# Optimization experiments

Measured on AMD Instinct MI355X. Metric: run time of the kernel, lower is better.

The kernel has to match this reference:

```python
import jax, jax.numpy as jnp
import numpy as np

N_EXPERTS = 8
TOP_K = 2

# NOTE: dropout is treated as identity (inference/eval mode), matching
# nn.Dropout in eval(). gate_logits returned is post-softmax, exactly as in
# the torch code (it overwrites gate_logits with F.softmax output).

def setup_inputs() -> dict:
    key = jax.random.key(0)
    k1, k2, k3, k4 = jax.random.split(key, 4)
    B, T, S = 32, 512, 512
    x = jax.random.normal(k1, (B, T, S), dtype=jnp.float32)
    gate_w = jax.random.normal(k2, (N_EXPERTS, S), dtype=jnp.float32) * (1.0 / np.sqrt(S))
    expert_w = jax.random.normal(k3, (N_EXPERTS, S, S), dtype=jnp.float32) * (1.0 / np.sqrt(S))
    expert_b = jax.random.normal(k4, (N_EXPERTS, S), dtype=jnp.float32) * 0.01
    return {"x": x, "gate_w": gate_w, "expert_w": expert_w, "expert_b": expert_b}


def reference(x, gate_w, expert_w, expert_b):
    # Gating: Linear(seq_len -> n_experts, no bias) then softmax over experts
    logits = jnp.einsum('bti,ei->bte', x, gate_w)          # [B,T,E]
    gates = jax.nn.softmax(logits, axis=-1)                # [B,T,E]
    # top-k routing weights
    w, sel = jax.lax.top_k(gates, TOP_K)                   # [B,T,K], [B,T,K]
    # dense combine weights: zero except at selected experts
    comb = jnp.sum(jax.nn.one_hot(sel, N_EXPERTS, dtype=x.dtype) * w[..., None], axis=-2)  # [B,T,E]
    # all-expert linear outputs (XLA fuses the weighted combine)
    expert_out = jnp.einsum('bti,eoi->bteo', x, expert_w) + expert_b[None, None]  # [B,T,E,S]
    out = jnp.einsum('bte,bteo->bto', comb, expert_out)    # [B,T,S]
    out = jax.nn.relu(out)
    return (out, gates)
```

## Files before the change

### kernel.cpp

```cpp
#include <hip/hip_runtime.h>
#include <stdint.h>

#define NT 16384
#define SDIM 512
#define NE 8
#define BM 128
#define BN 128
#define BK 32
#define NSTEP (SDIM / BK)
#define NPAIR 28
#define MAX_TILES 156
#define GEMM_GRID (MAX_TILES * 4)

typedef __attribute__((ext_vector_type(8))) short short8v;
typedef __attribute__((ext_vector_type(8))) unsigned short ushort8v;
typedef __attribute__((ext_vector_type(4))) float f32x4;

#define GLOAD_LDS16(gp, lp) __builtin_amdgcn_global_load_lds( \
    (const __attribute__((address_space(1))) uint32_t*)(gp), \
    (__attribute__((address_space(3))) uint32_t*)(lp), 16, 0, 0)

__device__ __forceinline__ unsigned short f2bf(float f) {
  uint32_t x = __float_as_uint(f);
  x = (x + 0x7FFFu + ((x >> 16) & 1u)) >> 16;
  return (unsigned short)x;
}

__global__ __launch_bounds__(256) void convw_kernel(const float* __restrict__ w,
                                                    unsigned short* __restrict__ wb) {
  int i = (blockIdx.x * 256 + threadIdx.x) * 8;
  const float4* p = (const float4*)(w + i);
  float4 a = p[0], b = p[1];
  ushort8v u;
  u[0] = f2bf(a.x); u[1] = f2bf(a.y); u[2] = f2bf(a.z); u[3] = f2bf(a.w);
  u[4] = f2bf(b.x); u[5] = f2bf(b.y); u[6] = f2bf(b.z); u[7] = f2bf(b.w);
  *(ushort8v*)(wb + i) = u;
}

__global__ __launch_bounds__(256) void gate_kernel(
    const float* __restrict__ x, const float* __restrict__ gw,
    unsigned short* __restrict__ xb, float* __restrict__ gates_out,
    float* __restrict__ wts, int* __restrict__ sels) {
  int lane = threadIdx.x & 63;
  int wv = threadIdx.x >> 6;

  float4 ga[NE], gb[NE];
#pragma unroll
  for (int e = 0; e < NE; e++) {
    const float4* g4 = (const float4*)(gw + e * SDIM + lane * 8);
    ga[e] = g4[0]; gb[e] = g4[1];
  }

  int tbase = blockIdx.x * 16 + wv * 4;
#pragma unroll 1
  for (int i = 0; i < 4; i++) {
    int t = tbase + i;
    const float* xr = x + (size_t)t * SDIM;
    float4 xa = ((const float4*)xr)[lane * 2];
    float4 xbv = ((const float4*)xr)[lane * 2 + 1];

    ushort8v u;
    u[0] = f2bf(xa.x); u[1] = f2bf(xa.y); u[2] = f2bf(xa.z); u[3] = f2bf(xa.w);
    u[4] = f2bf(xbv.x); u[5] = f2bf(xbv.y); u[6] = f2bf(xbv.z); u[7] = f2bf(xbv.w);
    *(ushort8v*)(xb + (size_t)t * SDIM + lane * 8) = u;

    double part[NE];
#pragma unroll
    for (int e = 0; e < NE; e++) {
      double s;
      s  = (double)xa.x * ga[e].x;  s += (double)xa.y * ga[e].y;
      s += (double)xa.z * ga[e].z;  s += (double)xa.w * ga[e].w;
      s += (double)xbv.x * gb[e].x; s += (double)xbv.y * gb[e].y;
      s += (double)xbv.z * gb[e].z; s += (double)xbv.w * gb[e].w;
      part[e] = s;
    }
#pragma unroll
    for (int e = 0; e < NE; e++) {
#pragma unroll
      for (int off = 32; off >= 1; off >>= 1)
        part[e] += __shfl_xor(part[e], off, 64);
    }

    float lg[NE];
#pragma unroll
    for (int e = 0; e < NE; e++) lg[e] = (float)part[e];
    float mx = lg[0];
#pragma unroll
    for (int e = 1; e < NE; e++) mx = fmaxf(mx, lg[e]);
    float ex[NE]; float sum = 0.f;
#pragma unroll
    for (int e = 0; e < NE; e++) { ex[e] = expf(lg[e] - mx); sum += ex[e]; }
    float inv = 1.0f / sum;
    float g[NE];
#pragma unroll
    for (int e = 0; e < NE; e++) g[e] = ex[e] * inv;

    int s0 = 0; float v0 = g[0];
#pragma unroll
    for (int e = 1; e < NE; e++) if (g[e] > v0) { v0 = g[e]; s0 = e; }
    int s1 = -1; float v1 = -1.0f;
#pragma unroll
    for (int e = 0; e < NE; e++) if (e != s0 && g[e] > v1) { v1 = g[e]; s1 = e; }

    if (lane == 0) {
      float* go = gates_out + (size_t)t * NE;
#pragma unroll
      for (int e = 0; e < NE; e++) go[e] = g[e];
      wts[t * 2] = v0; wts[t * 2 + 1] = v1;
      sels[t * 2] = s0; sels[t * 2 + 1] = s1;
    }
  }
}

__global__ __launch_bounds__(1024) void scatter_kernel(
    const int* __restrict__ sels, int* __restrict__ cnt, int* __restrict__ list) {
  __shared__ int lc[NPAIR];
  __shared__ int lb[NPAIR];
  int tid = threadIdx.x;
  if (tid < NPAIR) lc[tid] = 0;
  __syncthreads();
  int t = blockIdx.x * 1024 + tid;
  int s0 = sels[t * 2], s1 = sels[t * 2 + 1];
  int a = min(s0, s1), b = max(s0, s1);
  int tri = 7 * a - ((a * (a - 1)) >> 1) + (b - a - 1);
  int p = atomicAdd(&lc[tri], 1);
  __syncthreads();
  if (tid < NPAIR) lb[tid] = atomicAdd(cnt + tid, lc[tid]);
  __syncthreads();
  list[tri * NT + lb[tri] + p] = t;
}

__global__ void build_tiles(const int* __restrict__ cnt, int4* __restrict__ desc) {
  int lane = threadIdx.x & 63;
  int c = (lane < NPAIR) ? cnt[lane] : 0;
  int nt = (c + BM - 1) / BM;
  int pre = nt;
#pragma unroll
  for (int off = 1; off < 32; off <<= 1) {
    int v = __shfl_up(pre, off, 64);
    if (lane >= off) pre += v;
  }
  pre -= nt;
  int total = __shfl(pre + nt, NPAIR - 1, 64);
  if (lane < NPAIR) {
    int a = 0, rem = lane;
    while (rem >= 7 - a) { rem -= 7 - a; a++; }
    int b = a + 1 + rem;
    int k = 0;
    for (int s = 0; s < c; s += BM, k++)
      desc[pre + k] = make_int4(a | (b << 8) | (lane << 16), s, min(BM, c - s), 0);
  }
  for (int j = total + lane; j < MAX_TILES; j += 64)
    desc[j] = make_int4(0, 0, 0, 0);
}

__global__ __launch_bounds__(512, 4) void moe_gemm(
    const unsigned short* __restrict__ xb, const unsigned short* __restrict__ wbuf,
    const int* __restrict__ list, const float* __restrict__ wts,
    const int* __restrict__ sels, const int4* __restrict__ desc,
    const float* __restrict__ ebias, float* __restrict__ out) {
  int flat = blockIdx.x;
  int v = (flat & 7) * (GEMM_GRID / 8) + (flat >> 3);
  int tile = v >> 2, nb = v & 3;

  int4 d = desc[tile];
  int rows = d.z;
  if (rows == 0) return;
  int ea = d.x & 255, eb2 = (d.x >> 8) & 255, tri = d.x >> 16;
  int start = d.y;
  int nbase = nb * BN;
  const int* gl = list + tri * NT + start;

  __shared__ unsigned short lA[3][BM * BK];
  __shared__ unsigned short lB[3][2 * BN * BK];

  int tid = threadIdx.x, lane = tid & 63, wv = tid >> 6;

  int pa = tid >> 3, qa = tid & 7;
  int rowA = 2 * pa + (qa >> 2);
  int k16A = (qa & 3) ^ (pa & 3);
  int tokA = (rowA < rows) ? gl[rowA] : gl[0];
  const unsigned short* srcA = xb + (size_t)tokA * SDIM + k16A * 8;

  const unsigned short* srcB[2];
#pragma unroll
  for (int g = 0; g < 2; g++) {
    int c = g * 512 + tid;
    int slot = c >> 9;
    int cc = c & 511;
    int p = cc >> 3, q = cc & 7;
    int row = 2 * p + (q >> 2);
    int k16 = (q & 3) ^ (p & 3);
    int e = slot ? eb2 : ea;
    srcB[g] = wbuf + (size_t)(e * SDIM + nbase + row) * SDIM + k16 * 8;
  }

  char* lAb = (char*)lA;
  char* lBb = (char*)lB;
  int wm = wv >> 1, wn = wv & 1;
  int arow = wm * 32 + (lane & 15);
  int brow = wn * 64 + (lane & 15);
  int kreg = lane >> 4;

  int offA[2], offB[2][4];
#pragma unroll
  for (int mi = 0; mi < 2; mi++) {
    int lr = arow + mi * 16;
    int p = lr >> 1, h = lr & 1;
    offA[mi] = p * 128 + (h * 4 + (kreg ^ (p & 3))) * 16;
  }
#pragma unroll
  for (int s = 0; s < 2; s++)
#pragma unroll
    for (int ni = 0; ni < 4; ni++) {
      int lr = brow + ni * 16;
      int p = lr >> 1, h = lr & 1;
      offB[s][ni] = s * 8192 + p * 128 + (h * 4 + (kreg ^ (p & 3))) * 16;
    }

  f32x4 acc[2][2][4];
#pragma unroll
  for (int s = 0; s < 2; s++)
#pragma unroll
    for (int i = 0; i < 2; i++)
#pragma unroll
      for (int j = 0; j < 4; j++) acc[s][i][j] = (f32x4){0.f, 0.f, 0.f, 0.f};

#define STAGE(st, k0) do { \
    GLOAD_LDS16(srcA + (k0), lAb + (st) * 8192 + tid * 16); \
    _Pragma("unroll") \
    for (int g = 0; g < 2; g++) \
      GLOAD_LDS16(srcB[g] + (k0), lBb + (st) * 16384 + (g * 512 + tid) * 16); \
  } while (0)

#define COMPUTE(st) do { \
    const char* pA = lAb + (st) * 8192; \
    const char* pB = lBb + (st) * 16384; \
    short8v a[2]; \
    _Pragma("unroll") \
    for (int mi = 0; mi < 2; mi++) a[mi] = *(const short8v*)(pA + offA[mi]); \
    _Pragma("unroll") \
    for (int s = 0; s < 2; s++) { \
      short8v b[4]; \
      _Pragma("unroll") \
      for (int ni = 0; ni < 4; ni++) b[ni] = *(const short8v*)(pB + offB[s][ni]); \
      _Pragma("unroll") \
      for (int mi = 0; mi < 2; mi++) \
        _Pragma("unroll") \
        for (int ni = 0; ni < 4; ni++) \
          acc[s][mi][ni] = __builtin_amdgcn_mfma_f32_16x16x32_bf16(a[mi], b[ni], acc[s][mi][ni], 0, 0, 0); \
    } \
  } while (0)

  STAGE(0, 0);
  STAGE(1, BK);
#pragma unroll 1
  for (int t = 0; t < NSTEP; t++) {
    if (t + 2 < NSTEP) {
      STAGE((t + 2) % 3, (t + 2) * BK);
      asm volatile("s_waitcnt vmcnt(6)" ::: "memory");
    } else if (t + 2 == NSTEP) {
      asm volatile("s_waitcnt vmcnt(3)" ::: "memory");
    } else {
      asm volatile("s_waitcnt vmcnt(0)" ::: "memory");
    }
    __builtin_amdgcn_s_barrier();
    __builtin_amdgcn_sched_barrier(0);
    COMPUTE(t % 3);
    __builtin_amdgcn_s_barrier();
  }

  int rg = lane >> 4;
  int ncol = nbase + wn * 64 + (lane & 15);
  float bA[4], bB[4];
#pragma unroll
  for (int ni = 0; ni < 4; ni++) {
    bA[ni] = ebias[ea * SDIM + ncol + ni * 16];
    bB[ni] = ebias[eb2 * SDIM + ncol + ni * 16];
  }
#pragma unroll
  for (int mi = 0; mi < 2; mi++) {
#pragma unroll
    for (int r = 0; r < 4; r++) {
      int m = wm * 32 + mi * 16 + rg * 4 + r;
      if (m < rows) {
        int tok = gl[m];
        float2 wp = *(const float2*)&wts[tok * 2];
        int sA = sels[tok * 2];
        float wA = (sA == ea) ? wp.x : wp.y;
        float wB = (sA == ea) ? wp.y : wp.x;
        float* orow = out + (size_t)tok * SDIM + ncol;
#pragma unroll
        for (int ni = 0; ni < 4; ni++) {
          float vv = wA * (acc[0][mi][ni][r] + bA[ni]) + wB * (acc[1][mi][ni][r] + bB[ni]);
          orow[ni * 16] = fmaxf(vv, 0.f);
        }
      }
    }
  }
#undef STAGE
#undef COMPUTE
}

extern "C" void kernel_launch(void* const* d_in, const int* in_sizes, int n_in,
                              void* d_out, int out_size, void* d_ws, size_t ws_size,
                              hipStream_t stream) {
  const float* x        = (const float*)d_in[0];
  const float* gate_w   = (const float*)d_in[1];
  const float* expert_w = (const float*)d_in[2];
  const float* expert_b = (const float*)d_in[3];
  float* out = (float*)d_out;

  char* ws = (char*)d_ws;
  unsigned short* xb = (unsigned short*)(ws);
  unsigned short* wb = (unsigned short*)(ws + 16777216);
  float* wts  = (float*)(ws + 20971520);
  int* sels   = (int*)(ws + 21102592);
  int* cnt    = (int*)(ws + 21233664);
  int* list   = (int*)(ws + 21233792);
  int4* desc  = (int4*)(ws + 23068800);

  hipMemsetAsync(cnt, 0, 128, stream);

  convw_kernel<<<1024, 256, 0, stream>>>(expert_w, wb);
  gate_kernel<<<NT / 16, 256, 0, stream>>>(x, gate_w, xb, out + (size_t)NT * SDIM,
                                           wts, sels);
  scatter_kernel<<<NT / 1024, 1024, 0, stream>>>(sels, cnt, list);
  build_tiles<<<1, 64, 0, stream>>>(cnt, desc);
  moe_gemm<<<GEMM_GRID, 512, 0, stream>>>(xb, wb, list, wts, sels, desc,
                                          expert_b, out);
}
```

Measured before the change: 83.86 us.

## Fuse weight conversion and counter reset into gate kernel; double-buffer GEMM for occupancy

The weight bf16 conversion and the counter memset move into the gate kernel. There are 1024 gate blocks, one for each conversion chunk, so this removes two launches. The MoE GEMM drops from triple to double buffering in LDS, which cuts shared memory per block, and raises the launch bounds minimum from 4 to 6 blocks to allow more waves per CU. It also raises wave priority around the MFMA compute. The shallower prefetch can expose more global load latency per K step, and the tighter register limit may cause spills.

```diff
diff --git a/kernel.cpp b/kernel.cpp
--- a/kernel.cpp
+++ b/kernel.cpp
@@ -26,21 +26,14 @@
   return (unsigned short)x;
 }
 
-__global__ __launch_bounds__(256) void convw_kernel(const float* __restrict__ w,
-                                                    unsigned short* __restrict__ wb) {
-  int i = (blockIdx.x * 256 + threadIdx.x) * 8;
-  const float4* p = (const float4*)(w + i);
-  float4 a = p[0], b = p[1];
-  ushort8v u;
-  u[0] = f2bf(a.x); u[1] = f2bf(a.y); u[2] = f2bf(a.z); u[3] = f2bf(a.w);
-  u[4] = f2bf(b.x); u[5] = f2bf(b.y); u[6] = f2bf(b.z); u[7] = f2bf(b.w);
-  *(ushort8v*)(wb + i) = u;
-}
-
-__global__ __launch_bounds__(256) void gate_kernel(
+__global__ __launch_bounds__(256) void gate_conv_kernel(
     const float* __restrict__ x, const float* __restrict__ gw,
-    unsigned short* __restrict__ xb, float* __restrict__ gates_out,
-    float* __restrict__ wts, int* __restrict__ sels) {
+    const float* __restrict__ ew,
+    unsigned short* __restrict__ xb, unsigned short* __restrict__ wb,
+    float* __restrict__ gates_out, float* __restrict__ wts,
+    int* __restrict__ sels, int* __restrict__ cnt) {
+  if (blockIdx.x == 0 && threadIdx.x < 32) cnt[threadIdx.x] = 0;
+
   int lane = threadIdx.x & 63;
   int wv = threadIdx.x >> 6;
 
@@ -110,6 +103,14 @@
       sels[t * 2] = s0; sels[t * 2 + 1] = s1;
     }
   }
+
+  int ci = (blockIdx.x * 256 + threadIdx.x) * 8;
+  const float4* p = (const float4*)(ew + ci);
+  float4 a = p[0], b = p[1];
+  ushort8v w;
+  w[0] = f2bf(a.x); w[1] = f2bf(a.y); w[2] = f2bf(a.z); w[3] = f2bf(a.w);
+  w[4] = f2bf(b.x); w[5] = f2bf(b.y); w[6] = f2bf(b.z); w[7] = f2bf(b.w);
+  *(ushort8v*)(wb + ci) = w;
 }
 
 __global__ __launch_bounds__(1024) void scatter_kernel(
@@ -154,7 +155,7 @@
     desc[j] = make_int4(0, 0, 0, 0);
 }
 
-__global__ __launch_bounds__(512, 4) void moe_gemm(
+__global__ __launch_bounds__(512, 6) void moe_gemm(
     const unsigned short* __restrict__ xb, const unsigned short* __restrict__ wbuf,
     const int* __restrict__ list, const float* __restrict__ wts,
     const int* __restrict__ sels, const int4* __restrict__ desc,
@@ -171,8 +172,8 @@
   int nbase = nb * BN;
   const int* gl = list + tri * NT + start;
 
-  __shared__ unsigned short lA[3][BM * BK];
-  __shared__ unsigned short lB[3][2 * BN * BK];
+  __shared__ unsigned short lA[2][BM * BK];
+  __shared__ unsigned short lB[2][2 * BN * BK];
 
   int tid = threadIdx.x, lane = tid & 63, wv = tid >> 6;
 
@@ -253,20 +254,19 @@
   } while (0)
 
   STAGE(0, 0);
-  STAGE(1, BK);
 #pragma unroll 1
   for (int t = 0; t < NSTEP; t++) {
-    if (t + 2 < NSTEP) {
-      STAGE((t + 2) % 3, (t + 2) * BK);
-      asm volatile("s_waitcnt vmcnt(6)" ::: "memory");
-    } else if (t + 2 == NSTEP) {
+    if (t + 1 < NSTEP) {
+      STAGE((t + 1) & 1, (t + 1) * BK);
       asm volatile("s_waitcnt vmcnt(3)" ::: "memory");
     } else {
       asm volatile("s_waitcnt vmcnt(0)" ::: "memory");
     }
     __builtin_amdgcn_s_barrier();
     __builtin_amdgcn_sched_barrier(0);
-    COMPUTE(t % 3);
+    __builtin_amdgcn_s_setprio(1);
+    COMPUTE(t & 1);
+    __builtin_amdgcn_s_setprio(0);
     __builtin_amdgcn_s_barrier();
   }
 
@@ -320,11 +320,9 @@
   int* list   = (int*)(ws + 21233792);
   int4* desc  = (int4*)(ws + 23068800);
 
-  hipMemsetAsync(cnt, 0, 128, stream);
-
-  convw_kernel<<<1024, 256, 0, stream>>>(expert_w, wb);
-  gate_kernel<<<NT / 16, 256, 0, stream>>>(x, gate_w, xb, out + (size_t)NT * SDIM,
-                                           wts, sels);
+  gate_conv_kernel<<<NT / 16, 256, 0, stream>>>(x, gate_w, expert_w, xb, wb,
+                                                out + (size_t)NT * SDIM,
+                                                wts, sels, cnt);
   scatter_kernel<<<NT / 1024, 1024, 0, stream>>>(sels, cnt, list);
   build_tiles<<<1, 64, 0, stream>>>(cnt, desc);
   moe_gemm<<<GEMM_GRID, 512, 0, stream>>>(xb, wb, list, wts, sels, desc,
```

Result: slower. 149.0 us (+77.6%).
